# Performance work log

Measured on AMD Instinct MI355X. Metric: run time of the kernel, lower is better.

## Reference

```python
import jax, jax.numpy as jnp
import numpy as np

B, T, H = 4, 8192, 512
LN_EPS = 1e-5


def _ln(x, g, b):
    mu = jnp.mean(x, axis=-1, keepdims=True)
    var = jnp.mean((x - mu) ** 2, axis=-1, keepdims=True)
    return (x - mu) * jax.lax.rsqrt(var + LN_EPS) * g + b


def _log_g(x):
    # log of g(x) = x + 0.5 (x >= 0) else sigmoid(x); both branches NaN-safe.
    return jnp.where(x >= 0, jnp.log(jax.nn.relu(x) + 0.5), -jax.nn.softplus(-x))


def _min_gru(x, Wz, bz, Wh, bh):
    # minGRU parallel log-space scan ("Were RNNs All We Needed?" Alg.), h_0 = 0.
    k = x @ Wz + bz                      # [B,T,H] gate pre-activation
    log_z = -jax.nn.softplus(-k)         # log sigmoid(k)
    log_coeffs = -jax.nn.softplus(k)     # log (1 - sigmoid(k))
    log_tilde_h = _log_g(x @ Wh + bh)
    log_h0 = jnp.full((x.shape[0], 1, x.shape[2]), jnp.log(0.5), x.dtype)  # g(0)=0.5
    log_values = jnp.concatenate([log_h0, log_z + log_tilde_h], axis=1)   # [B,T+1,H]
    a_star = jnp.cumsum(jnp.pad(log_coeffs, ((0, 0), (1, 0), (0, 0))), axis=1)
    log_h = a_star + jax.lax.cumlogsumexp(log_values - a_star, axis=1)
    return jnp.exp(log_h)[:, 1:]         # drop h_0 slot -> [B,T,H]


def setup_inputs() -> dict:
    key = jax.random.key(0)
    ks = jax.random.split(key, 5)
    s = 1.0 / np.sqrt(H)
    return {
        "x": jax.random.normal(ks[0], (B, T, H), jnp.float32),
        "ln1_g": jnp.ones((H,), jnp.float32),
        "ln1_b": jnp.zeros((H,), jnp.float32),
        "Wz": jax.random.normal(ks[1], (H, H), jnp.float32) * s,
        "bz": jnp.zeros((H,), jnp.float32),
        "Wh": jax.random.normal(ks[2], (H, H), jnp.float32) * s,
        "bh": jnp.zeros((H,), jnp.float32),
        "ln2_g": jnp.ones((H,), jnp.float32),
        "ln2_b": jnp.zeros((H,), jnp.float32),
        "W1": jax.random.normal(ks[3], (H, H), jnp.float32) * s,
        "b1": jnp.zeros((H,), jnp.float32),
        "W2": jax.random.normal(ks[4], (H, H), jnp.float32) * s,
        "b2": jnp.zeros((H,), jnp.float32),
    }


def reference(x, ln1_g, ln1_b, Wz, bz, Wh, bh, ln2_g, ln2_b, W1, b1, W2, b2):
    # x = x + minGRU(ln_1(x))   (dropout=0 -> identity)
    x = x + _min_gru(_ln(x, ln1_g, ln1_b), Wz, bz, Wh, bh)
    # x = x + FFN(ln_2(x)) ; FFN = Linear -> ReLU -> Linear (hidden->hidden)
    h = jax.nn.relu(_ln(x, ln2_g, ln2_b) @ W1 + b1)
    x = x + (h @ W2 + b2)
    return x
```

## Files before the change

### kernel.cpp

```cpp
#include <hip/hip_runtime.h>

typedef unsigned short u16;
typedef unsigned int u32;
typedef __bf16 bf16x8 __attribute__((ext_vector_type(8)));
typedef float f32x4 __attribute__((ext_vector_type(4)));
typedef u16 u16x8 __attribute__((ext_vector_type(8)));

__device__ __forceinline__ u16 f2bf(float f) {
    union { float f; u32 i; } v; v.f = f;
    u32 x = v.i;
    u32 r = (x + 0x7fffu + ((x >> 16) & 1u)) >> 16;
    return (u16)r;
}
__device__ __forceinline__ float bf2f(u16 u) {
    union { u32 i; float f; } v; v.i = ((u32)u) << 16; return v.f;
}
__device__ __forceinline__ u16 f2h(float f) {
    union { _Float16 h; u16 u; } v; v.h = (_Float16)f; return v.u;
}
__device__ __forceinline__ float h2f(u16 u) {
    union { _Float16 h; u16 u; } v; v.u = u; return (float)v.h;
}

__device__ __forceinline__ void gld16(const void* g, void* l) {
    __builtin_amdgcn_global_load_lds(
        (const __attribute__((address_space(1))) void*)g,
        (__attribute__((address_space(3))) void*)l, 16, 0, 0);
}

__global__ __launch_bounds__(256) void prep(
    const float* __restrict__ x, const float* __restrict__ g,
    const float* __restrict__ b, u16* __restrict__ y,
    const float* __restrict__ w0, const float* __restrict__ w1,
    const float* __restrict__ w2, const float* __restrict__ w3,
    u16* __restrict__ d0, u16* __restrict__ d1,
    u16* __restrict__ d2, u16* __restrict__ d3)
{
    __shared__ u16 tl[32][33];
    if (blockIdx.x < 1024) {
        int bx = blockIdx.x;
        int mat = bx >> 8;
        int tile = bx & 255;
        int tx = (tile & 15) * 32;
        int ty = (tile >> 4) * 32;
        const float* src = (mat == 0) ? w0 : (mat == 1) ? w1 : (mat == 2) ? w2 : w3;
        u16* dst = (mat == 0) ? d0 : (mat == 1) ? d1 : (mat == 2) ? d2 : d3;
        int col = threadIdx.x & 31;
        int r8  = threadIdx.x >> 5;
        #pragma unroll
        for (int k = 0; k < 4; ++k) {
            int rr = r8 + k * 8;
            tl[rr][col] = f2bf(src[(ty + rr) * 512 + tx + col]);
        }
        __syncthreads();
        #pragma unroll
        for (int k = 0; k < 4; ++k) {
            int rr = r8 + k * 8;
            dst[(tx + rr) * 512 + ty + col] = tl[col][rr];
        }
        return;
    }
    int gid = (blockIdx.x - 1024) * 256 + threadIdx.x;
    int row = gid >> 6;
    int lane = gid & 63;

    const float* xr = x + (size_t)row * 512 + lane * 8;
    float4 a0 = *(const float4*)xr;
    float4 a1 = *(const float4*)(xr + 4);
    float f[8] = {a0.x, a0.y, a0.z, a0.w, a1.x, a1.y, a1.z, a1.w};
    float sm = 0.f, sm2 = 0.f;
    #pragma unroll
    for (int e = 0; e < 8; ++e) { sm += f[e]; sm2 += f[e] * f[e]; }
    #pragma unroll
    for (int o = 32; o > 0; o >>= 1) { sm += __shfl_xor(sm, o); sm2 += __shfl_xor(sm2, o); }
    const float inv = 1.0f / 512.0f;
    float mean = sm * inv;
    float var  = sm2 * inv - mean * mean;
    float rstd = rsqrtf(var + 1e-5f);

    float4 g0 = *(const float4*)(g + lane * 8);
    float4 g1 = *(const float4*)(g + lane * 8 + 4);
    float4 b0 = *(const float4*)(b + lane * 8);
    float4 b1 = *(const float4*)(b + lane * 8 + 4);
    float gg[8] = {g0.x, g0.y, g0.z, g0.w, g1.x, g1.y, g1.z, g1.w};
    float bb[8] = {b0.x, b0.y, b0.z, b0.w, b1.x, b1.y, b1.z, b1.w};
    u16x8 ov;
    #pragma unroll
    for (int e = 0; e < 8; ++e)
        ov[e] = f2bf((f[e] - mean) * rstd * gg[e] + bb[e]);
    *(u16x8*)(y + (size_t)row * 512 + lane * 8) = ov;
}

__global__ __launch_bounds__(256) void ln_k(
    const float* __restrict__ x, const float* __restrict__ g,
    const float* __restrict__ b, u16* __restrict__ y, int rows)
{
    int gid = blockIdx.x * blockDim.x + threadIdx.x;
    int row = gid >> 6;
    int lane = gid & 63;
    if (row >= rows) return;

    const float* xr = x + (size_t)row * 512 + lane * 8;
    float4 a0 = *(const float4*)xr;
    float4 a1 = *(const float4*)(xr + 4);
    float f[8] = {a0.x, a0.y, a0.z, a0.w, a1.x, a1.y, a1.z, a1.w};
    float sm = 0.f, sm2 = 0.f;
    #pragma unroll
    for (int e = 0; e < 8; ++e) { sm += f[e]; sm2 += f[e] * f[e]; }
    #pragma unroll
    for (int o = 32; o > 0; o >>= 1) { sm += __shfl_xor(sm, o); sm2 += __shfl_xor(sm2, o); }
    const float inv = 1.0f / 512.0f;
    float mean = sm * inv;
    float var  = sm2 * inv - mean * mean;
    float rstd = rsqrtf(var + 1e-5f);

    float4 g0 = *(const float4*)(g + lane * 8);
    float4 g1 = *(const float4*)(g + lane * 8 + 4);
    float4 b0 = *(const float4*)(b + lane * 8);
    float4 b1 = *(const float4*)(b + lane * 8 + 4);
    float gg[8] = {g0.x, g0.y, g0.z, g0.w, g1.x, g1.y, g1.z, g1.w};
    float bb[8] = {b0.x, b0.y, b0.z, b0.w, b1.x, b1.y, b1.z, b1.w};
    u16x8 ov;
    #pragma unroll
    for (int e = 0; e < 8; ++e)
        ov[e] = f2bf((f[e] - mean) * rstd * gg[e] + bb[e]);
    *(u16x8*)(y + (size_t)row * 512 + lane * 8) = ov;
}

__global__ __launch_bounds__(256, 2) void gemm_gate(
    const u16* __restrict__ A, const u16* __restrict__ Bt0,
    const u16* __restrict__ Bt1, const float* __restrict__ bias0,
    const float* __restrict__ bias1, u32* __restrict__ cvb,
    float* __restrict__ chCp, float* __restrict__ chVp)
{
    constexpr int Kd = 512, Nd = 512;
    constexpr int BUF = 12288;
    __shared__ __align__(16) u16 smem[2 * BUF];

    int bx = blockIdx.x;
    bx = (bx & 7) * 128 + (bx >> 3);
    int m0 = (bx >> 2) * 128;
    int n0 = (bx & 3) * 128;
    int tid = threadIdx.x;
    int lane = tid & 63;
    int w = tid >> 6;
    int wm = w & 1, wn = w >> 1;
    int l16 = lane & 15;
    int quad = lane >> 4;

    f32x4 acc0[4][4] = {};
    f32x4 acc1[4][4] = {};

    int ch0 = tid, ch1 = tid + 256;
    int row0 = ch0 >> 2, row1 = ch1 >> 2;
    int g0 = (ch0 & 3) ^ ((ch0 >> 3) & 3);
    int g1 = (ch1 & 3) ^ ((ch1 >> 3) & 3);
    const u16* a0p  = A   + (size_t)(m0 + row0) * Kd + g0 * 8;
    const u16* a1p  = A   + (size_t)(m0 + row1) * Kd + g1 * 8;
    const u16* b00p = Bt0 + (size_t)(n0 + row0) * Kd + g0 * 8;
    const u16* b01p = Bt0 + (size_t)(n0 + row1) * Kd + g1 * 8;
    const u16* b10p = Bt1 + (size_t)(n0 + row0) * Kd + g0 * 8;
    const u16* b11p = Bt1 + (size_t)(n0 + row1) * Kd + g1 * 8;

#define STAGE(sl, kt) { \
    int k0_ = (kt) * 32; \
    u16* L_ = smem + (sl) * BUF; \
    gld16(a0p  + k0_, &L_[ch0 * 8]); \
    gld16(a1p  + k0_, &L_[ch1 * 8]); \
    gld16(b00p + k0_, &L_[4096 + ch0 * 8]); \
    gld16(b01p + k0_, &L_[4096 + ch1 * 8]); \
    gld16(b10p + k0_, &L_[8192 + ch0 * 8]); \
    gld16(b11p + k0_, &L_[8192 + ch1 * 8]); }

    STAGE(0, 0);
    __syncthreads();

    for (int kt = 0; kt < Kd / 32; ++kt) {
        int cur = kt & 1;
        if (kt < Kd / 32 - 1) STAGE(cur ^ 1, kt + 1);

        const u16* As  = smem + cur * BUF;
        const u16* Bs0 = As + 4096;
        const u16* Bs1 = As + 8192;
        bf16x8 af[4], bf0[4], bf1[4];
        #pragma unroll
        for (int i = 0; i < 4; ++i) {
            int ra = wm * 64 + i * 16 + l16;
            int rb = wn * 64 + i * 16 + l16;
            int ga = quad ^ ((ra >> 1) & 3);
            int gb = quad ^ ((rb >> 1) & 3);
            af[i]  = *(const bf16x8*)&As [ra * 32 + ga * 8];
            bf0[i] = *(const bf16x8*)&Bs0[rb * 32 + gb * 8];
            bf1[i] = *(const bf16x8*)&Bs1[rb * 32 + gb * 8];
        }
        #pragma unroll
        for (int i = 0; i < 4; ++i)
            #pragma unroll
            for (int j = 0; j < 4; ++j) {
                acc0[i][j] = __builtin_amdgcn_mfma_f32_16x16x32_bf16(af[i], bf0[j], acc0[i][j], 0, 0, 0);
                acc1[i][j] = __builtin_amdgcn_mfma_f32_16x16x32_bf16(af[i], bf1[j], acc1[i][j], 0, 0, 0);
            }
        __syncthreads();
    }
#undef STAGE

    #pragma unroll
    for (int p = 0; p < 2; ++p) {
        int grow = m0 + wm * 64 + p * 32;
        int bb_  = grow >> 13;
        int chgl = (grow & 8191) >> 5;
        #pragma unroll
        for (int j = 0; j < 4; ++j) {
            int col = n0 + wn * 64 + j * 16 + l16;
            float bk  = bias0[col];
            float bh2 = bias1[col];
            float Cs[2], Vs[2];
            #pragma unroll
            for (int ii = 0; ii < 2; ++ii) {
                int i = 2 * p + ii;
                float C = 1.f, V = 0.f;
                #pragma unroll
                for (int r = 0; r < 4; ++r) {
                    int row = m0 + wm * 64 + i * 16 + quad * 4 + r;
                    float kk = acc0[i][j][r] + bk;
                    float hh = acc1[i][j][r] + bh2;
                    float z = __builtin_amdgcn_rcpf(1.f + __expf(-kk));
                    float c = 1.f - z;
                    float gs = __builtin_amdgcn_rcpf(1.f + __expf(-hh));
                    float gg = (hh >= 0.f) ? (hh + 0.5f) : gs;
                    float v = z * gg;
                    cvb[(size_t)row * Nd + col] =
                        (u32)f2h(c) | ((u32)f2h(v) << 16);
                    C *= c;
                    V = fmaf(c, V, v);
                }
                Cs[ii] = C; Vs[ii] = V;
            }
            #pragma unroll
            for (int ii = 0; ii < 2; ++ii) {
                float C = Cs[ii], V = Vs[ii];
                float oc = __shfl_xor(C, 16), ov = __shfl_xor(V, 16);
                V = (quad & 1) ? fmaf(C, ov, V) : fmaf(oc, V, ov);
                C *= oc;
                oc = __shfl_xor(C, 32); ov = __shfl_xor(V, 32);
                V = (quad & 2) ? fmaf(C, ov, V) : fmaf(oc, V, ov);
                C *= oc;
                Cs[ii] = C; Vs[ii] = V;
            }
            float Cch = Cs[0] * Cs[1];
            float Vch = fmaf(Cs[1], Vs[0], Vs[1]);
            if (quad == 0) {
                int idx = chgl * 2048 + bb_ * 512 + col;
                chCp[idx] = Cch;
                chVp[idx] = Vch;
            }
        }
    }
}

template <int MODE>
__global__ __launch_bounds__(256, 3) void gemm_bt(
    const u16* __restrict__ A, const u16* __restrict__ Bt0,
    const float* __restrict__ bias0, const float* __restrict__ resid,
    void* __restrict__ out0v)
{
    constexpr int Kd = 512, Nd = 512;
    constexpr int BUF = 8192;
    __shared__ __align__(16) u16 smem[2 * BUF];

    int bx = blockIdx.x;
    bx = (bx & 7) * 128 + (bx >> 3);
    int m0 = (bx >> 2) * 128;
    int n0 = (bx & 3) * 128;
    int tid = threadIdx.x;
    int lane = tid & 63;
    int w = tid >> 6;
    int wm = w & 1, wn = w >> 1;
    int l16 = lane & 15;
    int quad = lane >> 4;

    f32x4 acc0[4][4] = {};

    int ch0 = tid, ch1 = tid + 256;
    int row0 = ch0 >> 2, row1 = ch1 >> 2;
    int g0 = (ch0 & 3) ^ ((ch0 >> 3) & 3);
    int g1 = (ch1 & 3) ^ ((ch1 >> 3) & 3);
    const u16* a0p  = A   + (size_t)(m0 + row0) * Kd + g0 * 8;
    const u16* a1p  = A   + (size_t)(m0 + row1) * Kd + g1 * 8;
    const u16* b00p = Bt0 + (size_t)(n0 + row0) * Kd + g0 * 8;
    const u16* b01p = Bt0 + (size_t)(n0 + row1) * Kd + g1 * 8;

#define STAGE(sl, kt) { \
    int k0_ = (kt) * 32; \
    u16* L_ = smem + (sl) * BUF; \
    gld16(a0p  + k0_, &L_[ch0 * 8]); \
    gld16(a1p  + k0_, &L_[ch1 * 8]); \
    gld16(b00p + k0_, &L_[4096 + ch0 * 8]); \
    gld16(b01p + k0_, &L_[4096 + ch1 * 8]); }

    STAGE(0, 0);
    __syncthreads();

    for (int kt = 0; kt < Kd / 32; ++kt) {
        int cur = kt & 1;
        if (kt < Kd / 32 - 1) STAGE(cur ^ 1, kt + 1);

        const u16* As  = smem + cur * BUF;
        const u16* Bs0 = As + 4096;
        bf16x8 af[4], bf0[4];
        #pragma unroll
        for (int i = 0; i < 4; ++i) {
            int ra = wm * 64 + i * 16 + l16;
            int rb = wn * 64 + i * 16 + l16;
            int ga = quad ^ ((ra >> 1) & 3);
            int gb = quad ^ ((rb >> 1) & 3);
            af[i]  = *(const bf16x8*)&As [ra * 32 + ga * 8];
            bf0[i] = *(const bf16x8*)&Bs0[rb * 32 + gb * 8];
        }
        #pragma unroll
        for (int i = 0; i < 4; ++i)
            #pragma unroll
            for (int j = 0; j < 4; ++j)
                acc0[i][j] = __builtin_amdgcn_mfma_f32_16x16x32_bf16(af[i], bf0[j], acc0[i][j], 0, 0, 0);
        __syncthreads();
    }
#undef STAGE

    #pragma unroll
    for (int j = 0; j < 4; ++j) {
        int col = n0 + wn * 64 + j * 16 + l16;
        float b0 = bias0[col];
        #pragma unroll
        for (int i = 0; i < 4; ++i) {
            #pragma unroll
            for (int r = 0; r < 4; ++r) {
                int row = m0 + wm * 64 + i * 16 + quad * 4 + r;
                size_t off = (size_t)row * Nd + col;
                float v0 = acc0[i][j][r] + b0;
                if (MODE == 1) {
                    ((u16*)out0v)[off] = f2bf(fmaxf(v0, 0.f));
                } else {
                    ((float*)out0v)[off] = v0 + resid[off];
                }
            }
        }
    }
}

__global__ __launch_bounds__(256) void scanB(
    const float* __restrict__ chC, const float* __restrict__ chV,
    float* __restrict__ hst)
{
    int bx = blockIdx.x;
    int sc = bx >> 3;
    int s  = (bx & 7) * 256 + threadIdx.x;
    float h = 0.5f;
    int pre = sc * 16;
    #pragma unroll 8
    for (int c = 0; c < pre; ++c)
        h = fmaf(chC[c * 2048 + s], h, chV[c * 2048 + s]);
    #pragma unroll
    for (int i = 0; i < 16; ++i) {
        int ch = sc * 16 + i;
        hst[ch * 2048 + s] = h;
        h = fmaf(chC[ch * 2048 + s], h, chV[ch * 2048 + s]);
    }
}

__global__ __launch_bounds__(256) void scanC(
    const u32* __restrict__ cv, const float* __restrict__ hst,
    const float* __restrict__ x, float* __restrict__ x2)
{
    int gid = blockIdx.x * 256 + threadIdx.x;
    int h = gid & 511;
    int rest = gid >> 9;
    int b = rest & 3;
    int ch = rest >> 2;
    size_t base = ((size_t)(b * 8192 + ch * 32)) * 512 + h;
    float hc = hst[ch * 2048 + b * 512 + h];
    #pragma unroll 8
    for (int t = 0; t < 32; ++t) {
        size_t off = base + (size_t)t * 512;
        u32 g2 = cv[off];
        hc = fmaf(h2f((u16)(g2 & 0xffffu)), hc, h2f((u16)(g2 >> 16)));
        x2[off] = x[off] + hc;
    }
}

extern "C" void kernel_launch(void* const* d_in, const int* in_sizes, int n_in,
                              void* d_out, int out_size, void* d_ws, size_t ws_size,
                              hipStream_t stream)
{
    const float* x    = (const float*)d_in[0];
    const float* ln1g = (const float*)d_in[1];
    const float* ln1b = (const float*)d_in[2];
    const float* Wz   = (const float*)d_in[3];
    const float* bz   = (const float*)d_in[4];
    const float* Wh   = (const float*)d_in[5];
    const float* bh   = (const float*)d_in[6];
    const float* ln2g = (const float*)d_in[7];
    const float* ln2b = (const float*)d_in[8];
    const float* W1   = (const float*)d_in[9];
    const float* b1   = (const float*)d_in[10];
    const float* W2   = (const float*)d_in[11];
    const float* b2   = (const float*)d_in[12];
    float* out = (float*)d_out;

    char* ws = (char*)d_ws;
    constexpr size_t MB = 1024 * 1024;
    u16* Wzt = (u16*)(ws);
    u16* Wht = Wzt + 262144;
    u16* W1t = Wzt + 524288;
    u16* W2t = Wzt + 786432;
    u16* a   = (u16*)(ws + 3 * MB + 512 * 1024);
    u32* cv  = (u32*)(ws + 35 * MB + 512 * 1024);
    u16* hid = (u16*)(ws + 35 * MB + 512 * 1024);
    float* hst = (float*)(ws + 3 * MB + 512 * 1024);
    float* chC = (float*)d_out;
    float* chV = chC + 524288;

    prep<<<9216, 256, 0, stream>>>(x, ln1g, ln1b, a,
                                   Wz, Wh, W1, W2, Wzt, Wht, W1t, W2t);
    gemm_gate<<<1024, 256, 0, stream>>>(a, Wzt, Wht, bz, bh, cv, chC, chV);
    scanB<<<128, 256, 0, stream>>>(chC, chV, hst);
    scanC<<<2048, 256, 0, stream>>>(cv, hst, x, out);
    ln_k<<<8192, 256, 0, stream>>>(out, ln2g, ln2b, a, 32768);
    gemm_bt<1><<<1024, 256, 0, stream>>>(a, W1t, b1, nullptr, hid);
    gemm_bt<2><<<1024, 256, 0, stream>>>(hid, W2t, b2, out, out);
}
```

Baseline: 299.0 us.

## Fuse second LayerNorm into the scan-apply kernel and store chunk states in fp16

Result: slower. 309.1 us (+3.4%).

```diff
diff --git a/kernel.cpp b/kernel.cpp
--- a/kernel.cpp
+++ b/kernel.cpp
@@ -63,42 +63,6 @@
     int gid = (blockIdx.x - 1024) * 256 + threadIdx.x;
     int row = gid >> 6;
     int lane = gid & 63;
-
-    const float* xr = x + (size_t)row * 512 + lane * 8;
-    float4 a0 = *(const float4*)xr;
-    float4 a1 = *(const float4*)(xr + 4);
-    float f[8] = {a0.x, a0.y, a0.z, a0.w, a1.x, a1.y, a1.z, a1.w};
-    float sm = 0.f, sm2 = 0.f;
-    #pragma unroll
-    for (int e = 0; e < 8; ++e) { sm += f[e]; sm2 += f[e] * f[e]; }
-    #pragma unroll
-    for (int o = 32; o > 0; o >>= 1) { sm += __shfl_xor(sm, o); sm2 += __shfl_xor(sm2, o); }
-    const float inv = 1.0f / 512.0f;
-    float mean = sm * inv;
-    float var  = sm2 * inv - mean * mean;
-    float rstd = rsqrtf(var + 1e-5f);
-
-    float4 g0 = *(const float4*)(g + lane * 8);
-    float4 g1 = *(const float4*)(g + lane * 8 + 4);
-    float4 b0 = *(const float4*)(b + lane * 8);
-    float4 b1 = *(const float4*)(b + lane * 8 + 4);
-    float gg[8] = {g0.x, g0.y, g0.z, g0.w, g1.x, g1.y, g1.z, g1.w};
-    float bb[8] = {b0.x, b0.y, b0.z, b0.w, b1.x, b1.y, b1.z, b1.w};
-    u16x8 ov;
-    #pragma unroll
-    for (int e = 0; e < 8; ++e)
-        ov[e] = f2bf((f[e] - mean) * rstd * gg[e] + bb[e]);
-    *(u16x8*)(y + (size_t)row * 512 + lane * 8) = ov;
-}
-
-__global__ __launch_bounds__(256) void ln_k(
-    const float* __restrict__ x, const float* __restrict__ g,
-    const float* __restrict__ b, u16* __restrict__ y, int rows)
-{
-    int gid = blockIdx.x * blockDim.x + threadIdx.x;
-    int row = gid >> 6;
-    int lane = gid & 63;
-    if (row >= rows) return;
 
     const float* xr = x + (size_t)row * 512 + lane * 8;
     float4 a0 = *(const float4*)xr;
@@ -349,7 +313,7 @@
 
 __global__ __launch_bounds__(256) void scanB(
     const float* __restrict__ chC, const float* __restrict__ chV,
-    float* __restrict__ hst)
+    u16* __restrict__ hst)
 {
     int bx = blockIdx.x;
     int sc = bx >> 3;
@@ -362,28 +326,62 @@
     #pragma unroll
     for (int i = 0; i < 16; ++i) {
         int ch = sc * 16 + i;
-        hst[ch * 2048 + s] = h;
+        hst[ch * 2048 + s] = f2h(h);
         h = fmaf(chC[ch * 2048 + s], h, chV[ch * 2048 + s]);
     }
 }
 
-__global__ __launch_bounds__(256) void scanC(
-    const u32* __restrict__ cv, const float* __restrict__ hst,
-    const float* __restrict__ x, float* __restrict__ x2)
-{
-    int gid = blockIdx.x * 256 + threadIdx.x;
-    int h = gid & 511;
-    int rest = gid >> 9;
-    int b = rest & 3;
-    int ch = rest >> 2;
+__global__ __launch_bounds__(512) void scanC_ln(
+    const u32* __restrict__ cv, const u16* __restrict__ hst,
+    const float* __restrict__ x, const float* __restrict__ g,
+    const float* __restrict__ bia, float* __restrict__ x2,
+    u16* __restrict__ aout)
+{
+    __shared__ float sP[2][16][8], s2P[2][16][8];
+    int bx = blockIdx.x;
+    int b = bx >> 8;
+    int ch = bx & 255;
+    int h = threadIdx.x;
     size_t base = ((size_t)(b * 8192 + ch * 32)) * 512 + h;
-    float hc = hst[ch * 2048 + b * 512 + h];
-    #pragma unroll 8
-    for (int t = 0; t < 32; ++t) {
-        size_t off = base + (size_t)t * 512;
-        u32 g2 = cv[off];
-        hc = fmaf(h2f((u16)(g2 & 0xffffu)), hc, h2f((u16)(g2 >> 16)));
-        x2[off] = x[off] + hc;
+    float hc = h2f(hst[ch * 2048 + b * 512 + h]);
+    int lane = h & 63, wv = h >> 6;
+    const float inv = 1.0f / 512.0f;
+    float gg = g[h], bb = bia[h];
+    float xv[16];
+
+    #pragma unroll
+    for (int half = 0; half < 2; ++half) {
+        #pragma unroll
+        for (int t = 0; t < 16; ++t) {
+            size_t off = base + (size_t)(half * 16 + t) * 512;
+            u32 g2 = cv[off];
+            hc = fmaf(h2f((u16)(g2 & 0xffffu)), hc, h2f((u16)(g2 >> 16)));
+            float v = x[off] + hc;
+            xv[t] = v;
+            x2[off] = v;
+        }
+        #pragma unroll
+        for (int t = 0; t < 16; ++t) {
+            float s = xv[t], s2 = xv[t] * xv[t];
+            #pragma unroll
+            for (int o = 32; o > 0; o >>= 1) {
+                s += __shfl_xor(s, o);
+                s2 += __shfl_xor(s2, o);
+            }
+            if (lane == 0) { sP[half][t][wv] = s; s2P[half][t][wv] = s2; }
+        }
+        __syncthreads();
+        #pragma unroll
+        for (int t = 0; t < 16; ++t) {
+            float s = 0.f, s2 = 0.f;
+            #pragma unroll
+            for (int k = 0; k < 8; ++k) { s += sP[half][t][k]; s2 += s2P[half][t][k]; }
+            float mean = s * inv;
+            float var  = s2 * inv - mean * mean;
+            float rstd = rsqrtf(var + 1e-5f);
+            aout[base + (size_t)(half * 16 + t) * 512] =
+                f2bf((xv[t] - mean) * rstd * gg + bb);
+        }
     }
 }
 
@@ -412,10 +410,10 @@
     u16* Wht = Wzt + 262144;
     u16* W1t = Wzt + 524288;
     u16* W2t = Wzt + 786432;
+    u16* hst = (u16*)(ws + 2 * MB);
     u16* a   = (u16*)(ws + 3 * MB + 512 * 1024);
     u32* cv  = (u32*)(ws + 35 * MB + 512 * 1024);
     u16* hid = (u16*)(ws + 35 * MB + 512 * 1024);
-    float* hst = (float*)(ws + 3 * MB + 512 * 1024);
     float* chC = (float*)d_out;
     float* chV = chC + 524288;
 
@@ -423,8 +421,7 @@
                                    Wz, Wh, W1, W2, Wzt, Wht, W1t, W2t);
     gemm_gate<<<1024, 256, 0, stream>>>(a, Wzt, Wht, bz, bh, cv, chC, chV);
     scanB<<<128, 256, 0, stream>>>(chC, chV, hst);
-    scanC<<<2048, 256, 0, stream>>>(cv, hst, x, out);
-    ln_k<<<8192, 256, 0, stream>>>(out, ln2g, ln2b, a, 32768);
+    scanC_ln<<<1024, 512, 0, stream>>>(cv, hst, x, ln2g, ln2b, out, a);
     gemm_bt<1><<<1024, 256, 0, stream>>>(a, W1t, b1, nullptr, hid);
     gemm_bt<2><<<1024, 256, 0, stream>>>(hid, W2t, b2, out, out);
 }
```
